# Performance work log

Hardware: AMD Instinct MI355X
Metric: run time of the kernel (lower is better)

## Reference

```python
import jax, jax.numpy as jnp
import numpy as np

BIGNET_DIM = 1024
GROUP = 16
N_LIN = 15  # 6 blocks (last has no LN after) x 3 QLoRALinear
N_LN = 5
LORA_SCALE = 0.125  # 1/8
LN_EPS = 1e-5


def setup_inputs() -> dict:
    key = jax.random.key(0)
    ks = jax.random.split(key, 8)
    B = 8192
    x = jax.random.normal(ks[0], (B, BIGNET_DIM), dtype=jnp.float32)
    # 4-bit codes in [0, 16), group-wise fp16 scales (absmax-like, positive)
    q_w = jax.random.randint(ks[1], (N_LIN, BIGNET_DIM, BIGNET_DIM), 0, 16, dtype=jnp.int32)
    scales = (jax.random.uniform(ks[2], (N_LIN, BIGNET_DIM, BIGNET_DIM // GROUP)) * 0.05 + 0.01).astype(jnp.float16)
    biases = (jax.random.normal(ks[3], (N_LIN, BIGNET_DIM)) * 0.01).astype(jnp.float16)
    lora_A = jax.random.normal(ks[4], (N_LIN, 32, BIGNET_DIM), dtype=jnp.float32) * (1.0 / np.sqrt(BIGNET_DIM))
    # lora_B is zero-init in the module; use small random values so the LoRA path is exercised
    lora_B = jax.random.normal(ks[5], (N_LIN, BIGNET_DIM, 32), dtype=jnp.float32) * 0.01
    ln_g = jnp.ones((N_LN, BIGNET_DIM), dtype=jnp.float32)
    ln_b = jnp.zeros((N_LN, BIGNET_DIM), dtype=jnp.float32)
    return {"x": x, "q_w": q_w, "scales": scales, "biases": biases,
            "lora_A": lora_A, "lora_B": lora_B, "ln_g": ln_g, "ln_b": ln_b}


def _dequant4bit(q, scale):
    # q: [out, in] int codes in [0,16); scale: [out, in//GROUP] fp16
    # w = (q / 15 * 2 - 1) * group_scale, computed in fp16 like the torch code
    s = jnp.repeat(scale, GROUP, axis=1)  # [out, in]
    return (q.astype(jnp.float16) * jnp.float16(2.0 / 15.0) - jnp.float16(1.0)) * s


def _qlora_linear(x, q, scale, bias, A, B):
    w = _dequant4bit(q, scale)                                   # [out, in] f16
    half = jnp.dot(x.astype(jnp.float16), w.T) + bias            # f16 GEMM
    lora = jnp.dot(jnp.dot(x, A.T), B.T) * LORA_SCALE            # f32 rank-32 path
    return half.astype(jnp.float32) + lora


def _layernorm(x, g, b):
    mu = jnp.mean(x, axis=-1, keepdims=True)
    var = jnp.mean(jnp.square(x - mu), axis=-1, keepdims=True)
    return (x - mu) * jax.lax.rsqrt(var + LN_EPS) * g + b


def _forward(x, q_w, scales, biases, lora_A, lora_B, ln_g, ln_b):
    h = x
    li = 0
    for blk in range(6):
        r = h
        for j in range(3):
            r = _qlora_linear(r, q_w[li], scales[li], biases[li], lora_A[li], lora_B[li])
            li += 1
            if j < 2:
                r = jax.nn.relu(r)
        h = r + h  # block residual
        if blk < 5:
            h = _layernorm(h, ln_g[blk], ln_b[blk])
    return h


def reference(x, q_w, scales, biases, lora_A, lora_B, ln_g, ln_b):
    return _forward(x, q_w, scales, biases, lora_A, lora_B, ln_g, ln_b)
```

## Files before the change

kernel.cpp:

```cpp
#include <hip/hip_runtime.h>

typedef _Float16 f16;
typedef _Float16 f16x8 __attribute__((ext_vector_type(8)));
typedef _Float16 f16x4 __attribute__((ext_vector_type(4)));
typedef float f32x4 __attribute__((ext_vector_type(4)));


__global__ void detect_kernel(const unsigned short* __restrict__ sc, int* __restrict__ mode)
{
    if (threadIdx.x != 0 || blockIdx.x != 0) return;
    bool ok16 = true, okbf = true;
    for (int i = 0; i < 64; i++) {
        const unsigned short b = sc[i];
        union { unsigned short u; f16 h; } ch; ch.u = b;
        const float fv = (float)ch.h;
        if (!(fv > 0.008f && fv < 0.062f)) ok16 = false;
        union { unsigned int u; float f; } cb; cb.u = ((unsigned int)b) << 16;
        if (!(cb.f > 0.008f && cb.f < 0.062f)) okbf = false;
    }
    *mode = ok16 ? 0 : (okbf ? 1 : 2);
}

__device__ __forceinline__ float load_half_like(const void* p, int i, int mode)
{
    if (mode == 0) return (float)((const f16*)p)[i];
    if (mode == 1) {
        union { unsigned int u; float f; } c;
        c.u = ((unsigned int)((const unsigned short*)p)[i]) << 16;
        return c.f;
    }
    return ((const float*)p)[i];
}

__global__ void prep_kernel(const float* __restrict__ x, const int* __restrict__ qw,
                            const void* __restrict__ scales, const void* __restrict__ biases,
                            const float* __restrict__ lA, const float* __restrict__ lB,
                            const int* __restrict__ modep,
                            f16* __restrict__ Wdq, f16* __restrict__ A16,
                            f16* __restrict__ B16, f16* __restrict__ x16,
                            float* __restrict__ bias32)
{
    const int bid = blockIdx.x, tid = threadIdx.x;
    if (bid < 3840) {
        const int md = *modep;
        const int g = bid * 256 + tid;
        const float s = load_half_like(scales, g, md);
        const int4* qp = (const int4*)(qw + (size_t)g * 16);
        f16x8 w0, w1;
        #pragma unroll
        for (int v = 0; v < 4; v++) {
            const int4 q4 = qp[v];
            const int qs[4] = {q4.x, q4.y, q4.z, q4.w};
            #pragma unroll
            for (int j = 0; j < 4; j++) {
                f16 t = (f16)qs[j];
                t = t * (f16)(2.0f / 15.0f);
                t = t - (f16)1.0f;
                const f16 w = (f16)((float)t * s);
                if (v < 2) w0[v * 4 + j] = w; else w1[(v - 2) * 4 + j] = w;
            }
        }
        const int row = g >> 6;
        const int li  = row >> 10;
        const int col = row & 1023;
        const int grp = g & 63;
        const size_t dst = (size_t)li * 1048576 + (size_t)(grp >> 2) * 65536
                         + (size_t)col * 64 + ((grp & 3) << 4);
        *(f16x8*)(Wdq + dst) = w0;
        *(f16x8*)(Wdq + dst + 8) = w1;
    } else if (bid < 4320) {
        const int i = (bid - 3840) * 1024 + tid * 4;
        const float4 a = *(const float4*)(lA + i);
        f16x4 o = {(f16)a.x, (f16)a.y, (f16)a.z, (f16)a.w};
        const int li = i >> 15, j = i & 32767;
        const int p = j >> 10, k = j & 1023;
        *(f16x4*)(A16 + (size_t)li * 32768 + (size_t)(k >> 6) * 2048
                      + (size_t)p * 64 + (k & 63)) = o;
    } else if (bid < 4800) {
        const int i = (bid - 4320) * 1024 + tid * 4;
        const float4 a = *(const float4*)(lB + i);
        f16x4 o = {(f16)(0.125f * a.x), (f16)(0.125f * a.y),
                   (f16)(0.125f * a.z), (f16)(0.125f * a.w)};
        *(f16x4*)(B16 + i) = o;
    } else if (bid < 12992) {
        const int row = bid - 4800;
        const int k = tid * 4;
        const float4 a = *(const float4*)(x + (size_t)row * 1024 + k);
        f16x4 o = {(f16)a.x, (f16)a.y, (f16)a.z, (f16)a.w};
        *(f16x4*)(x16 + (size_t)(k >> 6) * 524288 + (size_t)row * 64 + (k & 63)) = o;
    } else {
        const int md = *modep;
        const int i = (bid - 12992) * 1024 + tid * 4;
        float4 o;
        o.x = load_half_like(biases, i, md);
        o.y = load_half_like(biases, i + 1, md);
        o.z = load_half_like(biases, i + 2, md);
        o.w = load_half_like(biases, i + 3, md);
        *(float4*)(bias32 + i) = o;
    }
}

__device__ __forceinline__ void gl_lds16(const f16* g, f16* l)
{
    __builtin_amdgcn_global_load_lds(
        (const __attribute__((address_space(1))) void*)g,
        (__attribute__((address_space(3))) void*)l, 16, 0, 0);
}

__global__ __launch_bounds__(256, 2)
void layer_kernel(const f16* __restrict__ X16, const f16* __restrict__ W,
                  const f16* __restrict__ AL, const f16* __restrict__ BL,
                  const float* __restrict__ biasL, const float* __restrict__ resid,
                  float* __restrict__ out32, f16* __restrict__ out16, int do_relu)
{
    __shared__ __align__(16) f16 lds[36864];

    const int tid  = threadIdx.x;
    const int lane = tid & 63;
    const int wv   = tid >> 6;
    const int wy   = wv >> 1, wx = wv & 1;
    const int by   = blockIdx.x & 63;
    const int bx   = blockIdx.x >> 6;
    const int row0 = by << 7;
    const int col0 = bx << 7;

    const int lr = lane >> 3;
    const int pc = lane & 7;
    const int csw = ((pc ^ lr) << 3);

    const int m15 = lane & 15;
    const int q2  = lane >> 4;
    const int sw  = m15 & 7;
    const int po0 = ((q2 ^ sw) << 3);
    const int po1 = (((4 + q2) ^ sw) << 3);
    const int q8  = q2 << 3;

    f32x4 acc[4][4] = {};
    f32x4 tacc[2][2] = {};

    auto stage = [&](f16* buf, int kt) {
        const f16* Xt = X16 + (size_t)kt * 524288 + csw;
        const f16* Wt = W   + (size_t)kt * 65536  + csw;
        const f16* At = AL  + (size_t)kt * 2048   + csw;
        #pragma unroll
        for (int i = 0; i < 4; i++) {
            gl_lds16(Xt + (size_t)(row0 + wv * 32 + i * 8 + lr) * 64,
                     buf + (wv * 32 + i * 8) * 64);
            gl_lds16(Wt + (size_t)(col0 + wv * 32 + i * 8 + lr) * 64,
                     buf + 8192 + (wv * 32 + i * 8) * 64);
        }
        gl_lds16(At + (size_t)(wv * 8 + lr) * 64,
                 buf + 16384 + wv * 8 * 64);
    };

    stage(lds, 0);

    for (int kt = 0; kt < 16; kt++) {
        __syncthreads();
        const f16* cur = lds + (kt & 1) * 18432;
        const f16* sA = cur;
        const f16* sB = cur + 8192;
        const f16* sL = cur + 16384;

        if (kt < 15) stage(lds + ((kt + 1) & 1) * 18432, kt + 1);

        f16x8 af[2][4], bf[2][4], lf[2][2];
        #pragma unroll
        for (int s = 0; s < 2; s++) {
            const int po = s ? po1 : po0;
            #pragma unroll
            for (int mi = 0; mi < 4; mi++)
                af[s][mi] = *(const f16x8*)(sA + (wy * 64 + mi * 16 + m15) * 64 + po);
            #pragma unroll
            for (int ni = 0; ni < 4; ni++)
                bf[s][ni] = *(const f16x8*)(sB + (wx * 64 + ni * 16 + m15) * 64 + po);
            #pragma unroll
            for (int pi = 0; pi < 2; pi++)
                lf[s][pi] = *(const f16x8*)(sL + (pi * 16 + m15) * 64 + po);
        }

        #pragma unroll
        for (int s = 0; s < 2; s++) {
            #pragma unroll
            for (int mi = 0; mi < 4; mi++)
                #pragma unroll
                for (int ni = 0; ni < 4; ni++)
                    acc[mi][ni] = __builtin_amdgcn_mfma_f32_16x16x32_f16(af[s][mi], bf[s][ni], acc[mi][ni], 0, 0, 0);
            #pragma unroll
            for (int mi = 0; mi < 2; mi++)
                #pragma unroll
                for (int pi = 0; pi < 2; pi++)
                    tacc[mi][pi] = __builtin_amdgcn_mfma_f32_16x16x32_f16(af[s][2 * wx + mi], lf[s][pi], tacc[mi][pi], 0, 0, 0);
        }
    }

    __syncthreads();
    float* Tl = (float*)lds;
    const int q4 = (lane >> 4) << 2;
    {
        #pragma unroll
        for (int mi = 0; mi < 2; mi++)
            #pragma unroll
            for (int pi = 0; pi < 2; pi++)
                #pragma unroll
                for (int r = 0; r < 4; r++)
                    Tl[(wy * 64 + wx * 32 + mi * 16 + q4 + r) * 33 + pi * 16 + m15] = tacc[mi][pi][r];
    }
    __syncthreads();

    f16x8 tf[4];
    #pragma unroll
    for (int mi = 0; mi < 4; mi++) {
        const float* tp = Tl + (wy * 64 + mi * 16 + m15) * 33 + q8;
        f16x8 v;
        #pragma unroll
        for (int j = 0; j < 8; j++) v[j] = (f16)tp[j];
        tf[mi] = v;
    }
    f16x8 bfr[4]; float bb[4];
    #pragma unroll
    for (int ni = 0; ni < 4; ni++) {
        const int colg = col0 + wx * 64 + ni * 16 + m15;
        bfr[ni] = *(const f16x8*)(BL + (size_t)colg * 32 + q8);
        bb[ni] = biasL[colg];
    }
    #pragma unroll
    for (int mi = 0; mi < 4; mi++)
        #pragma unroll
        for (int ni = 0; ni < 4; ni++) {
            #pragma unroll
            for (int r = 0; r < 4; r++)
                acc[mi][ni][r] += bb[ni];
            acc[mi][ni] = __builtin_amdgcn_mfma_f32_16x16x32_f16(tf[mi], bfr[ni], acc[mi][ni], 0, 0, 0);
        }

    __syncthreads();
    if (out16) {
        f16* ot = lds;
        #pragma unroll
        for (int mi = 0; mi < 4; mi++)
            #pragma unroll
            for (int ni = 0; ni < 4; ni++)
                #pragma unroll
                for (int r = 0; r < 4; r++) {
                    float v = acc[mi][ni][r];
                    if (do_relu) v = fmaxf(v, 0.0f);
                    ot[(wy * 64 + mi * 16 + q4 + r) * 136 + wx * 64 + ni * 16 + m15] = (f16)v;
                }
        __syncthreads();
        const int rr = tid >> 4;
        const int cc = (tid & 15) << 3;
        f16* o0 = out16 + (size_t)(2 * bx + (cc >> 6)) * 524288 + (cc & 63);
        #pragma unroll
        for (int it = 0; it < 8; it++) {
            const int r = it * 16 + rr;
            const f16x8 v = *(const f16x8*)(ot + r * 136 + cc);
            *(f16x8*)(o0 + (size_t)(row0 + r) * 64) = v;
        }
    } else {
        float* otf = (float*)lds;
        const int rr = tid >> 5;
        const int cc = (tid & 31) << 2;
        #pragma unroll
        for (int half = 0; half < 2; half++) {
            if (wy == half) {
                #pragma unroll
                for (int mi = 0; mi < 4; mi++)
                    #pragma unroll
                    for (int ni = 0; ni < 4; ni++)
                        #pragma unroll
                        for (int r = 0; r < 4; r++)
                            otf[(mi * 16 + q4 + r) * 140 + wx * 64 + ni * 16 + m15] = acc[mi][ni][r];
            }
            __syncthreads();
            #pragma unroll
            for (int it = 0; it < 8; it++) {
                const int r = it * 8 + rr;
                f32x4 v = *(const f32x4*)(otf + r * 140 + cc);
                const size_t gidx = (size_t)(row0 + half * 64 + r) * 1024 + col0 + cc;
                const f32x4 rs = *(const f32x4*)(resid + gidx);
                v += rs;
                *(f32x4*)(out32 + gidx) = v;
            }
            if (half == 0) __syncthreads();
        }
    }
}

__global__ void ln_kernel(float* __restrict__ h, f16* __restrict__ h16,
                          const float* __restrict__ g, const float* __restrict__ b)
{
    const int row = blockIdx.x, tid = threadIdx.x;
    float* hp = h + (size_t)row * 1024;
    const int c = tid * 4;
    const float4 v = *(const float4*)(hp + c);
    float s = v.x + v.y + v.z + v.w;
    #pragma unroll
    for (int off = 32; off > 0; off >>= 1) s += __shfl_down(s, off);
    __shared__ float r1[4], r2[4];
    const int wv = tid >> 6, lane = tid & 63;
    if (lane == 0) r1[wv] = s;
    __syncthreads();
    const float mu = (r1[0] + r1[1] + r1[2] + r1[3]) * (1.0f / 1024.0f);
    const float dx = v.x - mu, dy = v.y - mu, dz = v.z - mu, dw = v.w - mu;
    float s2 = dx * dx + dy * dy + dz * dz + dw * dw;
    #pragma unroll
    for (int off = 32; off > 0; off >>= 1) s2 += __shfl_down(s2, off);
    if (lane == 0) r2[wv] = s2;
    __syncthreads();
    const float var = (r2[0] + r2[1] + r2[2] + r2[3]) * (1.0f / 1024.0f);
    const float rs = 1.0f / sqrtf(var + 1e-5f);
    float4 o;
    o.x = dx * rs * g[c]     + b[c];
    o.y = dy * rs * g[c + 1] + b[c + 1];
    o.z = dz * rs * g[c + 2] + b[c + 2];
    o.w = dw * rs * g[c + 3] + b[c + 3];
    *(float4*)(hp + c) = o;
    f16x4 o16 = {(f16)o.x, (f16)o.y, (f16)o.z, (f16)o.w};
    *(f16x4*)(h16 + (size_t)(c >> 6) * 524288 + (size_t)row * 64 + (c & 63)) = o16;
}

extern "C" void kernel_launch(void* const* d_in, const int* in_sizes, int n_in,
                              void* d_out, int out_size, void* d_ws, size_t ws_size,
                              hipStream_t stream)
{
    const float* x      = (const float*)d_in[0];
    const int*   qw     = (const int*)d_in[1];
    const void*  scales = d_in[2];
    const void*  biases = d_in[3];
    const float* lA     = (const float*)d_in[4];
    const float* lB     = (const float*)d_in[5];
    const float* lng    = (const float*)d_in[6];
    const float* lnb    = (const float*)d_in[7];
    float* out = (float*)d_out;

    char* ws = (char*)d_ws;
    int*   mode   = (int*)(ws);
    float* bias32 = (float*)(ws + 64);
    f16* Wdq = (f16*)(ws + 65536u);
    f16* A16 = (f16*)(ws + 31522816u);
    f16* B16 = (f16*)(ws + 32505856u);
    f16* fA  = (f16*)(ws + 33488896u);
    f16* fB  = (f16*)(ws + 50266112u);
    float* h32 = out;

    detect_kernel<<<1, 64, 0, stream>>>((const unsigned short*)scales, mode);
    prep_kernel<<<13007, 256, 0, stream>>>(x, qw, scales, biases, lA, lB, mode,
                                           Wdq, A16, B16, fA, bias32);

    int li = 0;
    for (int blk = 0; blk < 6; blk++) {
        const float* resid = (blk == 0) ? x : h32;
        for (int j = 0; j < 3; j++, li++) {
            const int wl = li < 15 ? li : 14;
            const f16* in16 = (j == 1) ? fB : fA;
            f16* o16 = (j == 0) ? fB : (j == 1 ? fA : (f16*)nullptr);
            float* o32 = nullptr;
            const float* rz = nullptr;
            if (j == 2) { o32 = h32; rz = resid; }
            layer_kernel<<<512, 256, 0, stream>>>(in16,
                Wdq + (size_t)wl * 1048576,
                A16 + (size_t)wl * 32768,
                B16 + (size_t)wl * 32768,
                bias32 + (size_t)wl * 1024,
                rz, o32, o16, j < 2 ? 1 : 0);
        }
        if (blk < 5)
            ln_kernel<<<8192, 256, 0, stream>>>(h32, fA, lng + blk * 1024, lnb + blk * 1024);
    }
}
```

Baseline: 1.383 ms.

## Use 256x128 tiles with 8 waves and halve K-step to 32

The layer GEMM now uses 512-thread blocks covering 256 rows by 128 columns, so each weight tile is reused across twice as many rows, and the grid shrinks from 512 to 256 blocks. The K loop now advances by 32 per stage instead of 64, which cuts the LDS footprint per buffer and doubles the number of iterations and barriers. The epilogues are rewritten to stage output in smaller LDS chunks with more synchronisation steps. The grid is only 256 blocks, which may underfill the device's compute units, and each K step does less MFMA work per barrier.

```diff
diff --git a/kernel.cpp b/kernel.cpp
--- a/kernel.cpp
+++ b/kernel.cpp
@@ -107,96 +107,89 @@
         (__attribute__((address_space(3))) void*)l, 16, 0, 0);
 }
 
-__global__ __launch_bounds__(256, 2)
+__global__ __launch_bounds__(512, 1)
 void layer_kernel(const f16* __restrict__ X16, const f16* __restrict__ W,
                   const f16* __restrict__ AL, const f16* __restrict__ BL,
                   const float* __restrict__ biasL, const float* __restrict__ resid,
                   float* __restrict__ out32, f16* __restrict__ out16, int do_relu)
 {
-    __shared__ __align__(16) f16 lds[36864];
+    __shared__ __align__(16) f16 lds[26624];
 
     const int tid  = threadIdx.x;
     const int lane = tid & 63;
     const int wv   = tid >> 6;
-    const int wy   = wv >> 1, wx = wv & 1;
-    const int by   = blockIdx.x & 63;
-    const int bx   = blockIdx.x >> 6;
-    const int row0 = by << 7;
+    const int wy   = wv >> 1;
+    const int wx   = wv & 1;
+    const int by   = blockIdx.x & 31;
+    const int bx   = blockIdx.x >> 5;
+    const int row0 = by << 8;
     const int col0 = bx << 7;
 
-    const int lr = lane >> 3;
-    const int pc = lane & 7;
-    const int csw = ((pc ^ lr) << 3);
+    const int lr4 = lane >> 2;
+    const int csw = (((lane & 3) ^ (lr4 & 3)) << 3);
 
     const int m15 = lane & 15;
     const int q2  = lane >> 4;
-    const int sw  = m15 & 7;
-    const int po0 = ((q2 ^ sw) << 3);
-    const int po1 = (((4 + q2) ^ sw) << 3);
+    const int po  = ((q2 ^ (m15 & 3)) << 3);
     const int q8  = q2 << 3;
 
     f32x4 acc[4][4] = {};
     f32x4 tacc[2][2] = {};
 
-    auto stage = [&](f16* buf, int kt) {
-        const f16* Xt = X16 + (size_t)kt * 524288 + csw;
-        const f16* Wt = W   + (size_t)kt * 65536  + csw;
-        const f16* At = AL  + (size_t)kt * 2048   + csw;
-        #pragma unroll
-        for (int i = 0; i < 4; i++) {
-            gl_lds16(Xt + (size_t)(row0 + wv * 32 + i * 8 + lr) * 64,
-                     buf + (wv * 32 + i * 8) * 64);
-            gl_lds16(Wt + (size_t)(col0 + wv * 32 + i * 8 + lr) * 64,
-                     buf + 8192 + (wv * 32 + i * 8) * 64);
-        }
-        gl_lds16(At + (size_t)(wv * 8 + lr) * 64,
-                 buf + 16384 + wv * 8 * 64);
+    auto stage = [&](f16* buf, int ks) {
+        const int kt64 = ks >> 1;
+        const int kb   = ((ks & 1) << 5) + csw;
+        const f16* Xt = X16 + (size_t)kt64 * 524288;
+        const f16* Wt = W   + (size_t)kt64 * 65536;
+        const f16* At = AL  + (size_t)kt64 * 2048;
+        #pragma unroll
+        for (int i = 0; i < 2; i++)
+            gl_lds16(Xt + (size_t)(row0 + wv * 32 + i * 16 + lr4) * 64 + kb,
+                     buf + (wv * 32 + i * 16) * 32);
+        gl_lds16(Wt + (size_t)(col0 + wv * 16 + lr4) * 64 + kb,
+                 buf + 8192 + (wv * 16) * 32);
+        if (wv < 2)
+            gl_lds16(At + (size_t)(wv * 16 + lr4) * 64 + kb,
+                     buf + 12288 + (wv * 16) * 32);
     };
 
     stage(lds, 0);
 
-    for (int kt = 0; kt < 16; kt++) {
+    for (int ks = 0; ks < 32; ks++) {
         __syncthreads();
-        const f16* cur = lds + (kt & 1) * 18432;
+        const f16* cur = lds + (ks & 1) * 13312;
         const f16* sA = cur;
         const f16* sB = cur + 8192;
-        const f16* sL = cur + 16384;
-
-        if (kt < 15) stage(lds + ((kt + 1) & 1) * 18432, kt + 1);
-
-        f16x8 af[2][4], bf[2][4], lf[2][2];
-        #pragma unroll
-        for (int s = 0; s < 2; s++) {
-            const int po = s ? po1 : po0;
-            #pragma unroll
-            for (int mi = 0; mi < 4; mi++)
-                af[s][mi] = *(const f16x8*)(sA + (wy * 64 + mi * 16 + m15) * 64 + po);
+        const f16* sL = cur + 12288;
+
+        if (ks < 31) stage(lds + ((ks + 1) & 1) * 13312, ks + 1);
+
+        f16x8 af[4], bf[4], lf[2];
+        #pragma unroll
+        for (int mi = 0; mi < 4; mi++)
+            af[mi] = *(const f16x8*)(sA + (wy * 64 + mi * 16 + m15) * 32 + po);
+        #pragma unroll
+        for (int ni = 0; ni < 4; ni++)
+            bf[ni] = *(const f16x8*)(sB + (wx * 64 + ni * 16 + m15) * 32 + po);
+        #pragma unroll
+        for (int pi = 0; pi < 2; pi++)
+            lf[pi] = *(const f16x8*)(sL + (pi * 16 + m15) * 32 + po);
+
+        #pragma unroll
+        for (int mi = 0; mi < 4; mi++)
             #pragma unroll
             for (int ni = 0; ni < 4; ni++)
-                bf[s][ni] = *(const f16x8*)(sB + (wx * 64 + ni * 16 + m15) * 64 + po);
+                acc[mi][ni] = __builtin_amdgcn_mfma_f32_16x16x32_f16(af[mi], bf[ni], acc[mi][ni], 0, 0, 0);
+        #pragma unroll
+        for (int mi = 0; mi < 2; mi++)
             #pragma unroll
             for (int pi = 0; pi < 2; pi++)
-                lf[s][pi] = *(const f16x8*)(sL + (pi * 16 + m15) * 64 + po);
-        }
-
-        #pragma unroll
-        for (int s = 0; s < 2; s++) {
-            #pragma unroll
-            for (int mi = 0; mi < 4; mi++)
-                #pragma unroll
-                for (int ni = 0; ni < 4; ni++)
-                    acc[mi][ni] = __builtin_amdgcn_mfma_f32_16x16x32_f16(af[s][mi], bf[s][ni], acc[mi][ni], 0, 0, 0);
-            #pragma unroll
-            for (int mi = 0; mi < 2; mi++)
-                #pragma unroll
-                for (int pi = 0; pi < 2; pi++)
-                    tacc[mi][pi] = __builtin_amdgcn_mfma_f32_16x16x32_f16(af[s][2 * wx + mi], lf[s][pi], tacc[mi][pi], 0, 0, 0);
-        }
+                tacc[mi][pi] = __builtin_amdgcn_mfma_f32_16x16x32_f16(af[2 * wx + mi], lf[pi], tacc[mi][pi], 0, 0, 0);
     }
 
     __syncthreads();
     float* Tl = (float*)lds;
-    const int q4 = (lane >> 4) << 2;
+    const int q4 = q2 << 2;
     {
         #pragma unroll
         for (int mi = 0; mi < 2; mi++)
@@ -238,51 +231,56 @@
     if (out16) {
         f16* ot = lds;
         #pragma unroll
-        for (int mi = 0; mi < 4; mi++)
-            #pragma unroll
-            for (int ni = 0; ni < 4; ni++)
+        for (int p = 0; p < 2; p++) {
+            if (wx == p) {
                 #pragma unroll
-                for (int r = 0; r < 4; r++) {
-                    float v = acc[mi][ni][r];
-                    if (do_relu) v = fmaxf(v, 0.0f);
-                    ot[(wy * 64 + mi * 16 + q4 + r) * 136 + wx * 64 + ni * 16 + m15] = (f16)v;
-                }
-        __syncthreads();
-        const int rr = tid >> 4;
-        const int cc = (tid & 15) << 3;
-        f16* o0 = out16 + (size_t)(2 * bx + (cc >> 6)) * 524288 + (cc & 63);
-        #pragma unroll
-        for (int it = 0; it < 8; it++) {
-            const int r = it * 16 + rr;
-            const f16x8 v = *(const f16x8*)(ot + r * 136 + cc);
-            *(f16x8*)(o0 + (size_t)(row0 + r) * 64) = v;
+                for (int mi = 0; mi < 4; mi++)
+                    #pragma unroll
+                    for (int ni = 0; ni < 4; ni++)
+                        #pragma unroll
+                        for (int r = 0; r < 4; r++) {
+                            float v = acc[mi][ni][r];
+                            if (do_relu) v = fmaxf(v, 0.0f);
+                            ot[(wy * 64 + mi * 16 + q4 + r) * 72 + ni * 16 + m15] = (f16)v;
+                        }
+            }
+            __syncthreads();
+            f16* op = out16 + (size_t)(2 * bx + p) * 524288 + (size_t)row0 * 64;
+            const int rr = tid >> 3;
+            const int cc = (tid & 7) << 3;
+            #pragma unroll
+            for (int it = 0; it < 4; it++) {
+                const int r = it * 64 + rr;
+                *(f16x8*)(op + (size_t)r * 64 + cc) = *(const f16x8*)(ot + r * 72 + cc);
+            }
+            if (p == 0) __syncthreads();
         }
     } else {
         float* otf = (float*)lds;
-        const int rr = tid >> 5;
-        const int cc = (tid & 31) << 2;
-        #pragma unroll
-        for (int half = 0; half < 2; half++) {
-            if (wy == half) {
+        #pragma unroll
+        for (int q = 0; q < 4; q++) {
+            if (wy == q) {
                 #pragma unroll
                 for (int mi = 0; mi < 4; mi++)
                     #pragma unroll
                     for (int ni = 0; ni < 4; ni++)
                         #pragma unroll
                         for (int r = 0; r < 4; r++)
-                            otf[(mi * 16 + q4 + r) * 140 + wx * 64 + ni * 16 + m15] = acc[mi][ni][r];
+                            otf[(mi * 16 + q4 + r) * 132 + wx * 64 + ni * 16 + m15] = acc[mi][ni][r];
             }
             __syncthreads();
-            #pragma unroll
-            for (int it = 0; it < 8; it++) {
-                const int r = it * 8 + rr;
-                f32x4 v = *(const f32x4*)(otf + r * 140 + cc);
-                const size_t gidx = (size_t)(row0 + half * 64 + r) * 1024 + col0 + cc;
+            const int rr = tid >> 5;
+            const int cc = (tid & 31) << 2;
+            #pragma unroll
+            for (int it = 0; it < 4; it++) {
+                const int r = it * 16 + rr;
+                f32x4 v = *(const f32x4*)(otf + r * 132 + cc);
+                const size_t gidx = (size_t)(row0 + q * 64 + r) * 1024 + col0 + cc;
                 const f32x4 rs = *(const f32x4*)(resid + gidx);
                 v += rs;
                 *(f32x4*)(out32 + gidx) = v;
             }
-            if (half == 0) __syncthreads();
+            if (q < 3) __syncthreads();
         }
     }
 }
@@ -358,7 +356,7 @@
             float* o32 = nullptr;
             const float* rz = nullptr;
             if (j == 2) { o32 = h32; rz = resid; }
-            layer_kernel<<<512, 256, 0, stream>>>(in16,
+            layer_kernel<<<256, 512, 0, stream>>>(in16,
                 Wdq + (size_t)wl * 1048576,
                 A16 + (size_t)wl * 32768,
                 B16 + (size_t)wl * 32768,
```

New measurement: 2.687 ms. +94.2%, slower.
